# Kernel optimization log

Measured on AMD Instinct MI355X. Metric: run time of the kernel, lower is better.

## Reference

```python
import jax, jax.numpy as jnp
import numpy as np


def setup_inputs() -> dict:
    key = jax.random.key(0)
    k_tok, k_lp = jax.random.split(key)
    R, S, V = 512, 1024, 50257  # rows = bsz*beam, seq_len, vocab
    tokens = jax.random.randint(k_tok, (R, S), 0, V, dtype=jnp.int64)
    lprobs = jax.random.normal(k_lp, (R, V), dtype=jnp.float32)
    return {
        "tokens": tokens,
        "lprobs": lprobs,
        "bsz": 128,
        "step": 1020,
        "beam_size": 4,
        "no_repeat_ngram_size": 3,
    }


def reference(tokens, lprobs, bsz, step, beam_size, no_repeat_ngram_size):
    # Semantics of fairseq's ngram_repeat_block CUDA kernel:
    # for each row, if tokens[row, i:i+n-1] == tokens[row, step-n+2:step+1]
    # for any window start i in [0, step-n+1], ban token tokens[row, i+n-1].
    n = no_repeat_ngram_size
    R = tokens.shape[0]
    V = lprobs.shape[1]
    num_windows = step - n + 2  # static Python int

    last = tokens[:, step - n + 2 : step + 1]            # (R, n-1) final (n-1)-gram
    starts = jnp.arange(num_windows)
    win_idx = starts[:, None] + jnp.arange(n - 1)[None, :]  # (W, n-1)
    prefixes = tokens[:, win_idx]                        # (R, W, n-1)
    match = jnp.all(prefixes == last[:, None, :], axis=-1)  # (R, W) bool
    banned = tokens[:, starts + (n - 1)]                 # (R, W) tokens to ban

    # Scatter -inf into matched banned positions; unmatched windows point
    # out-of-range (index V) and are dropped.
    scatter_idx = jnp.where(match, banned, V)            # (R, W)
    rows = jnp.arange(R)[:, None]
    return lprobs.at[rows, scatter_idx].set(-jnp.inf, mode="drop")
```

## Files before the change

kernel.cpp:

```cpp
#include <hip/hip_runtime.h>
#include <math.h>

__global__ void __launch_bounds__(256)
ngram_copy(const float4* __restrict__ in4, float4* __restrict__ out4,
           const float* __restrict__ in, float* __restrict__ out,
           int n4, int tail) {
    int i = blockIdx.x * 256 + threadIdx.x;
    if (i < n4) out4[i] = in4[i];
    if (blockIdx.x == 0 && threadIdx.x < tail) {
        int t = n4 * 4 + threadIdx.x;
        out[t] = in[t];
    }
}

__global__ void __launch_bounds__(256)
ngram_ban(const int* __restrict__ tokens, float* __restrict__ out,
          const int* __restrict__ bsz_p, const int* __restrict__ step_p,
          const int* __restrict__ beam_p, const int* __restrict__ n_p,
          long long tok_elems, long long lp_elems) {
    const int bsz  = *bsz_p;
    const int step = *step_p;
    const int beam = *beam_p;
    const int n    = *n_p;

    const int R = bsz * beam;
    const long long S = tok_elems / R;
    const long long V = lp_elems / R;
    const int num_windows = step - n + 2;
    const int last_start  = step - n + 2;
    const int L = n - 1;

    for (int r = blockIdx.x; r < R; r += gridDim.x) {
        const int* __restrict__ trow = tokens + (long long)r * S;
        for (int j = threadIdx.x; j < num_windows; j += blockDim.x) {
            bool m = true;
            for (int k = 0; k < L; ++k) {
                m &= (trow[j + k] == trow[last_start + k]);
            }
            if (m) {
                const int banned = trow[j + n - 1];
                out[(long long)r * V + banned] = -INFINITY;
            }
        }
    }
}

extern "C" void kernel_launch(void* const* d_in, const int* in_sizes, int n_in,
                              void* d_out, int out_size, void* d_ws, size_t ws_size,
                              hipStream_t stream) {
    const int*   tokens = (const int*)d_in[0];
    const float* lprobs = (const float*)d_in[1];
    const int*   bsz_p  = (const int*)d_in[2];
    const int*   step_p = (const int*)d_in[3];
    const int*   beam_p = (const int*)d_in[4];
    const int*   n_p    = (const int*)d_in[5];
    float* out = (float*)d_out;

    {
        const int n4   = out_size / 4;
        const int tail = out_size - n4 * 4;
        const int blocks = (n4 + 255) / 256;
        ngram_copy<<<blocks, 256, 0, stream>>>(
            (const float4*)lprobs, (float4*)out, lprobs, out, n4, tail);
    }

    {
        const int blocks = 512;
        ngram_ban<<<blocks, 256, 0, stream>>>(
            tokens, out, bsz_p, step_p, beam_p, n_p,
            (long long)in_sizes[0], (long long)in_sizes[1]);
    }
}
```

Baseline: 191.5 us.

## Fuse lprobs copy and n-gram ban into one chunked kernel

Replaces the separate copy kernel and ban kernel with a single kernel. Each block copies a contiguous chunk of lprobs, then scans only the token rows whose vocab range overlaps that chunk. Matching bans are collected in shared memory and written after a block barrier, so they land after the copy of the same addresses. This drops the second launch and the serial dependency between the two kernels, at the cost of each row's window scan being repeated by every block that touches that row.

Measured after the change: 196.9 us. 1.03x slower.

```diff
diff --git a/kernel.cpp b/kernel.cpp
--- a/kernel.cpp
+++ b/kernel.cpp
@@ -1,23 +1,36 @@
 #include <hip/hip_runtime.h>
 #include <math.h>
 
-__global__ void __launch_bounds__(256)
-ngram_copy(const float4* __restrict__ in4, float4* __restrict__ out4,
-           const float* __restrict__ in, float* __restrict__ out,
-           int n4, int tail) {
-    int i = blockIdx.x * 256 + threadIdx.x;
-    if (i < n4) out4[i] = in4[i];
-    if (blockIdx.x == 0 && threadIdx.x < tail) {
-        int t = n4 * 4 + threadIdx.x;
-        out[t] = in[t];
-    }
-}
+
+#define CHUNK4   2048
+#define MAX_BANS 2048
 
 __global__ void __launch_bounds__(256)
-ngram_ban(const int* __restrict__ tokens, float* __restrict__ out,
-          const int* __restrict__ bsz_p, const int* __restrict__ step_p,
-          const int* __restrict__ beam_p, const int* __restrict__ n_p,
-          long long tok_elems, long long lp_elems) {
+ngram_fused(const float4* __restrict__ in4, float4* __restrict__ out4,
+            const float* __restrict__ in, float* __restrict__ out,
+            const int* __restrict__ tokens,
+            const int* __restrict__ bsz_p, const int* __restrict__ step_p,
+            const int* __restrict__ beam_p, const int* __restrict__ n_p,
+            long long tok_elems, int total_f, int n4) {
+    __shared__ int s_cnt;
+    __shared__ int s_ban[MAX_BANS];
+
+    const int b  = blockIdx.x;
+    const int t  = threadIdx.x;
+    const int lo4 = b * CHUNK4;
+    const int hi4 = (lo4 + CHUNK4 < n4) ? lo4 + CHUNK4 : n4;
+
+    if (t == 0) s_cnt = 0;
+    __syncthreads();
+
+    for (int i = lo4 + t; i < hi4; i += 256) {
+        out4[i] = in4[i];
+    }
+    if (b == gridDim.x - 1) {
+        int tf = n4 * 4 + t;
+        if (tf < total_f) out[tf] = in[tf];
+    }
+
     const int bsz  = *bsz_p;
     const int step = *step_p;
     const int beam = *beam_p;
@@ -25,23 +38,40 @@
 
     const int R = bsz * beam;
     const long long S = tok_elems / R;
-    const long long V = lp_elems / R;
+    const int V = total_f / R;
     const int num_windows = step - n + 2;
     const int last_start  = step - n + 2;
     const int L = n - 1;
 
-    for (int r = blockIdx.x; r < R; r += gridDim.x) {
+    const int flo = lo4 * 4;
+    const int fhi = (b == gridDim.x - 1) ? total_f : hi4 * 4;
+
+    const int r0 = flo / V;
+    const int r1 = (fhi - 1) / V;
+
+    for (int r = r0; r <= r1; ++r) {
         const int* __restrict__ trow = tokens + (long long)r * S;
-        for (int j = threadIdx.x; j < num_windows; j += blockDim.x) {
+        const int rbase = r * V;
+        for (int j = t; j < num_windows; j += 256) {
             bool m = true;
             for (int k = 0; k < L; ++k) {
                 m &= (trow[j + k] == trow[last_start + k]);
             }
             if (m) {
                 const int banned = trow[j + n - 1];
-                out[(long long)r * V + banned] = -INFINITY;
+                const int f = rbase + banned;
+                if (f >= flo && f < fhi) {
+                    int idx = atomicAdd(&s_cnt, 1);
+                    if (idx < MAX_BANS) s_ban[idx] = f - flo;
+                }
             }
         }
+    }
+
+    __syncthreads();
+    const int cnt = (s_cnt < MAX_BANS) ? s_cnt : MAX_BANS;
+    for (int i = t; i < cnt; i += 256) {
+        out[flo + s_ban[i]] = -INFINITY;
     }
 }
 
@@ -56,18 +86,12 @@
     const int*   n_p    = (const int*)d_in[5];
     float* out = (float*)d_out;
 
-    {
-        const int n4   = out_size / 4;
-        const int tail = out_size - n4 * 4;
-        const int blocks = (n4 + 255) / 256;
-        ngram_copy<<<blocks, 256, 0, stream>>>(
-            (const float4*)lprobs, (float4*)out, lprobs, out, n4, tail);
-    }
+    const int total_f = out_size;
+    const int n4      = total_f / 4;
+    const int blocks  = (n4 + CHUNK4 - 1) / CHUNK4;
 
-    {
-        const int blocks = 512;
-        ngram_ban<<<blocks, 256, 0, stream>>>(
-            tokens, out, bsz_p, step_p, beam_p, n_p,
-            (long long)in_sizes[0], (long long)in_sizes[1]);
-    }
+    ngram_fused<<<blocks, 256, 0, stream>>>(
+        (const float4*)lprobs, (float4*)out, lprobs, out,
+        tokens, bsz_p, step_p, beam_p, n_p,
+        (long long)in_sizes[0], total_f, n4);
 }
```
